# Kernel tuning notes

Hardware: AMD Instinct MI355X
Metric: run time of the kernel (lower is better)

## Reference

```python
import jax, jax.numpy as jnp
import numpy as np


def setup_inputs() -> dict:
    key = jax.random.key(0)
    k_v, k_w = jax.random.split(key)
    L, N, H, D = 2048, 8, 16, 64
    v = jax.random.normal(k_v, (N, L, H, D), dtype=jnp.float32)
    # torch init: self.w.data.uniform_(-0.1, 0.1) overwrites the sorted randn
    w = jax.random.uniform(k_w, (L,), dtype=jnp.float32, minval=-0.1, maxval=0.1)
    return {"v": v, "w": w}


def _toeplitz_bias(w):
    # Faithful to _construnct_bias: p = [flip(w[1:]), w], bias[i, j] = p[L-1 - i + j]
    # which is the symmetric Toeplitz matrix bias[i, j] = w[|i - j|].
    L = w.shape[0]
    idx = jnp.abs(jnp.arange(L)[:, None] - jnp.arange(L)[None, :])  # [L, L]
    return w[idx]


def reference(v, w):
    # PositionalBias._naive
    L = w.shape[0]
    bias = _toeplitz_bias(w)                      # [L, L]
    z_pb = bias.sum(-1).reshape(1, L, 1)          # [1, L, 1]
    pbv = jnp.einsum('nlhd,lj->njhd', v, bias)    # [N, L, H, D]
    return pbv, z_pb
```

## Files before the change

kernel.cpp:

```cpp
#include <hip/hip_runtime.h>
#include <hip/hip_bf16.h>

#define L 2048
#define HD 1024
#define NB 8
#define NT 32
#define PROW 4096

using f32x4 = __attribute__((ext_vector_type(4))) float;
using fl4   = __attribute__((ext_vector_type(4))) float;
using s16x8 = __attribute__((ext_vector_type(8))) short;

__device__ __forceinline__ short f2bf(float f) {
    __hip_bfloat16 h = __float2bfloat16(f);
    short s;
    __builtin_memcpy(&s, &h, 2);
    return s;
}

__device__ __forceinline__ void gload_lds16(const void* g, void* l) {
    __builtin_amdgcn_global_load_lds(
        (const __attribute__((address_space(1))) unsigned int*)g,
        (__attribute__((address_space(3))) unsigned int*)l, 16, 0, 0);
}

__global__ __launch_bounds__(256) void pb_prep(const float* __restrict__ w,
                                               short* __restrict__ p8) {
    int idx = blockIdx.x * 256 + threadIdx.x;
    int s = idx >> 12;
    int x = idx & (PROW - 1);
    int k = x + s;
    short val = 0;
    if (k <= 4094) {
        int d = k - 2047; d = d < 0 ? -d : d;
        val = f2bf(w[d]);
    }
    p8[idx] = val;
}

__global__ __launch_bounds__(256) void pb_vtile(const float* __restrict__ v,
                                                s16x8* __restrict__ vtile) {
    __shared__ __align__(16) short Ts[256 * 64];
    const int kk = blockIdx.x, cm = blockIdx.y, n = blockIdx.z;
    const int l0 = kk * 64, c0 = cm * 256;
    const int t = threadIdx.x;
    const float* vn = v + (size_t)n * L * HD;

    #pragma unroll
    for (int i = 0; i < 16; ++i) {
        int unit = i * 256 + t;
        int l = unit >> 6, cq = unit & 63;
        fl4 x = *(const fl4*)&vn[(size_t)(l0 + l) * HD + c0 + cq * 4];
        int lsub = l & 7, lblk = l >> 3;
        #pragma unroll
        for (int j = 0; j < 4; ++j) {
            int c = cq * 4 + j;
            Ts[c * 64 + ((lblk ^ ((c >> 2) & 7)) << 3) + lsub] = f2bf(x[j]);
        }
    }
    __syncthreads();

    s16x8* outtile = vtile + ((size_t)((n * 4 + cm) * NT + kk)) * 2048;
    #pragma unroll
    for (int i2 = 0; i2 < 8; ++i2) {
        int ci = i2 * 256 + t;
        int nh = ci >> 10, cih = ci & 1023;
        int seg = cih >> 8, o = cih & 255;
        int c = seg * 64 + nh * 32 + (o >> 3), s = o & 7;
        int h = s ^ (c & 7);
        int slot = h ^ ((c >> 2) & 7);
        outtile[ci] = *(const s16x8*)&Ts[c * 64 + slot * 8];
    }
}

__global__ __launch_bounds__(512, 2) void pb_gemm8(const short* __restrict__ p8,
                                                   const short* __restrict__ vtile,
                                                   float* __restrict__ out) {
    __shared__ __align__(16) short lds_[65536];

    const int bid = blockIdx.x;
    const int cmn = bid & 31;
    const int jm  = bid >> 5;
    const int cm  = cmn & 3;
    const int n   = cmn >> 2;
    const int j0 = jm * 256;
    const int c0 = cm * 256;

    const int t = threadIdx.x;
    const int lane = t & 63;
    const int w = t >> 6;
    const int wr = w >> 2, wc = w & 3;
    const int fr = lane & 15, fk = lane >> 4;

    int offA[8], offB[4];
    #pragma unroll
    for (int m = 0; m < 8; ++m) {
        int r = wr * 128 + m * 16 + fr;
        offA[m] = r * 128 + ((fk ^ (r & 7)) << 4);
    }
    #pragma unroll
    for (int nf = 0; nf < 4; ++nf) {
        int c = wc * 64 + nf * 16 + fr;
        offB[nf] = c * 128 + ((fk ^ (c & 7)) << 4);
    }

    auto mkA = [&](int mh, int rho) {
        int dc = rho * 1024 + mh * 512 + w * 64 + lane;
        int r = dc >> 3, s = dc & 7, h = s ^ (r & 7);
        int q = 2047 + h * 8 - j0 - r;
        int srow = q & 7;
        return p8 + srow * PROW + (q - srow);
    };
    const short* srcA0_0 = mkA(0, 0); const short* srcA0_1 = mkA(0, 1);
    const short* srcA1_0 = mkA(1, 0); const short* srcA1_1 = mkA(1, 1);

    const short* vb = vtile + ((size_t)((n * 4 + cm) * NT)) * 2048 * 8;
    const short* srcB0_0 = vb + ((w) * 64 + lane) * 8;
    const short* srcB0_1 = vb + ((w + 8) * 64 + lane) * 8;
    const short* srcB1_0 = vb + (1024 + (w) * 64 + lane) * 8;
    const short* srcB1_1 = vb + (1024 + (w + 8) * 64 + lane) * 8;

    const int dA0 = w * 1024, dA1 = 16384 + w * 1024;
    const int dB0 = 32768 + (w >> 2) * 8192 + (w & 3) * 1024;
    const int dB1 = dB0 + 16384;

#define STAGE_A0(base) { gload_lds16(srcA0_0, (char*)lds_ + (base) + dA0); \
                         gload_lds16(srcA0_1, (char*)lds_ + (base) + dA1); \
                         srcA0_0 += 64; srcA0_1 += 64; }
#define STAGE_A1(base) { gload_lds16(srcA1_0, (char*)lds_ + (base) + 8192 + dA0); \
                         gload_lds16(srcA1_1, (char*)lds_ + (base) + 8192 + dA1); \
                         srcA1_0 += 64; srcA1_1 += 64; }
#define STAGE_B0(base) { gload_lds16(srcB0_0, (char*)lds_ + (base) + dB0); \
                         gload_lds16(srcB0_1, (char*)lds_ + (base) + dB1); \
                         srcB0_0 += 16384; srcB0_1 += 16384; }
#define STAGE_B1(base) { gload_lds16(srcB1_0, (char*)lds_ + (base) + 4096 + dB0); \
                         gload_lds16(srcB1_1, (char*)lds_ + (base) + 4096 + dB1); \
                         srcB1_0 += 16384; srcB1_1 += 16384; }
#define BAR()    asm volatile("s_barrier" ::: "memory")
#define LGKM0()  { asm volatile("s_waitcnt lgkmcnt(0)" ::: "memory"); \
                   __builtin_amdgcn_sched_barrier(0); }
#define VMC4()   asm volatile("s_waitcnt vmcnt(4)" ::: "memory")
#define VMC0()   asm volatile("s_waitcnt vmcnt(0)" ::: "memory")

    STAGE_A0(0); STAGE_A1(0); STAGE_B0(0); STAGE_B1(0);
    STAGE_A0(65536); STAGE_B0(65536);
    VMC4();
    BAR();

    f32x4 acc[8][4] = {};
    s16x8 af[4][2], bf0[2][2], bf1[2][2];

    for (int T = 0; T < NT; ++T) {
        const int par = T & 1;
        const char* bR = (const char*)lds_ + par * 65536;
        const int dstN = (par ^ 1) * 65536;
        const int dstC = par * 65536;

        #pragma unroll
        for (int m = 0; m < 4; ++m) {
            af[m][0] = *(const s16x8*)(bR + offA[m]);
            af[m][1] = *(const s16x8*)(bR + (offA[m] ^ 64));
        }
        #pragma unroll
        for (int nf = 0; nf < 2; ++nf) {
            bf0[nf][0] = *(const s16x8*)(bR + 32768 + offB[nf]);
            bf0[nf][1] = *(const s16x8*)(bR + 32768 + (offB[nf] ^ 64));
        }
        if (T < NT - 1) { STAGE_A1(dstN); }
        BAR(); LGKM0();
        __builtin_amdgcn_s_setprio(1);
        #pragma unroll
        for (int m = 0; m < 4; ++m)
            #pragma unroll
            for (int nf = 0; nf < 2; ++nf)
                #pragma unroll
                for (int ki = 0; ki < 2; ++ki)
                    acc[m][nf] = __builtin_amdgcn_mfma_f32_16x16x32_bf16(
                        af[m][ki], bf0[nf][ki], acc[m][nf], 0, 0, 0);
        __builtin_amdgcn_s_setprio(0);
        BAR();

        #pragma unroll
        for (int nf = 0; nf < 2; ++nf) {
            bf1[nf][0] = *(const s16x8*)(bR + 32768 + offB[2 + nf]);
            bf1[nf][1] = *(const s16x8*)(bR + 32768 + (offB[2 + nf] ^ 64));
        }
        if (T < NT - 1) { STAGE_B1(dstN); }
        BAR(); LGKM0();
        __builtin_amdgcn_s_setprio(1);
        #pragma unroll
        for (int m = 0; m < 4; ++m)
            #pragma unroll
            for (int nf = 0; nf < 2; ++nf)
                #pragma unroll
                for (int ki = 0; ki < 2; ++ki)
                    acc[m][2 + nf] = __builtin_amdgcn_mfma_f32_16x16x32_bf16(
                        af[m][ki], bf1[nf][ki], acc[m][2 + nf], 0, 0, 0);
        __builtin_amdgcn_s_setprio(0);
        BAR();

        #pragma unroll
        for (int m = 0; m < 4; ++m) {
            af[m][0] = *(const s16x8*)(bR + offA[4 + m]);
            af[m][1] = *(const s16x8*)(bR + (offA[4 + m] ^ 64));
        }
        if (T < NT - 2) { STAGE_A0(dstC); }
        BAR(); LGKM0();
        __builtin_amdgcn_s_setprio(1);
        #pragma unroll
        for (int m = 0; m < 4; ++m)
            #pragma unroll
            for (int nf = 0; nf < 2; ++nf)
                #pragma unroll
                for (int ki = 0; ki < 2; ++ki)
                    acc[4 + m][nf] = __builtin_amdgcn_mfma_f32_16x16x32_bf16(
                        af[m][ki], bf0[nf][ki], acc[4 + m][nf], 0, 0, 0);
        __builtin_amdgcn_s_setprio(0);
        BAR();

        if (T < NT - 2) { STAGE_B0(dstC); VMC4(); }
        else            { VMC0(); }
        BAR(); LGKM0();
        __builtin_amdgcn_s_setprio(1);
        #pragma unroll
        for (int m = 0; m < 4; ++m)
            #pragma unroll
            for (int nf = 0; nf < 2; ++nf)
                #pragma unroll
                for (int ki = 0; ki < 2; ++ki)
                    acc[4 + m][2 + nf] = __builtin_amdgcn_mfma_f32_16x16x32_bf16(
                        af[m][ki], bf1[nf][ki], acc[4 + m][2 + nf], 0, 0, 0);
        __builtin_amdgcn_s_setprio(0);
        BAR();
    }

    float* outn = out + (size_t)n * L * HD;
    #pragma unroll
    for (int m = 0; m < 8; ++m) {
        const int row = j0 + wr * 128 + m * 16 + fk * 4;
        #pragma unroll
        for (int nf = 0; nf < 4; ++nf) {
            const int col = c0 + wc * 64 + nf * 16 + fr;
            #pragma unroll
            for (int r = 0; r < 4; ++r)
                outn[(size_t)(row + r) * HD + col] = acc[m][nf][r];
        }
    }
}

__global__ __launch_bounds__(256) void pb_z(const float* __restrict__ w,
                                            float* __restrict__ z) {
    __shared__ float part[256];
    __shared__ float S[L];
    const int t = threadIdx.x;
    float loc[8]; float s = 0.f;
    #pragma unroll
    for (int i = 0; i < 8; ++i) { loc[i] = w[t * 8 + i]; s += loc[i]; }
    part[t] = s;
    __syncthreads();
    if (t == 0) {
        float a = 0.f;
        for (int i = 0; i < 256; ++i) { float tmp = part[i]; part[i] = a; a += tmp; }
    }
    __syncthreads();
    float a = part[t];
    #pragma unroll
    for (int i = 0; i < 8; ++i) { a += loc[i]; S[t * 8 + i] = a; }
    __syncthreads();
    const float w0 = S[0];
    #pragma unroll
    for (int i = 0; i < 8; ++i) {
        int j = t * 8 + i;
        z[j] = S[j] + S[2047 - j] - w0;
    }
}

extern "C" void kernel_launch(void* const* d_in, const int* in_sizes, int n_in,
                              void* d_out, int out_size, void* d_ws, size_t ws_size,
                              hipStream_t stream) {
    const float* v = (const float*)d_in[0];
    const float* w = (const float*)d_in[1];
    float* out = (float*)d_out;

    short* p8    = (short*)d_ws;
    short* vtile = (short*)((char*)d_ws + 65536);

    pb_prep<<<128, 256, 0, stream>>>(w, p8);
    pb_vtile<<<dim3(NT, 4, NB), 256, 0, stream>>>(v, (s16x8*)vtile);
    pb_gemm8<<<256, 512, 0, stream>>>(p8, vtile, out);
    pb_z<<<1, 256, 0, stream>>>(w, out + (size_t)NB * L * HD);
}
```

Baseline: 87.39 us.

## Replace phased LDS pipeline with simple whole-tile double buffering

Drops the four-phase schedule, in which each quarter of the next tile was staged between MFMA groups under explicit barriers, lgkmcnt/vmcnt waits and s_setprio. The new loop issues all eight async global-to-LDS loads for the next tile at the top of each iteration, runs all MFMAs, and ends with a single __syncthreads. This cuts the barrier count per iteration from eight to one and simplifies the code. The cost is coarser overlap, lost wave prioritisation, and reliance on __syncthreads to wait for the async LDS loads to finish.

Result: faster. 81.58 us (-6.6%).

```diff
diff --git a/kernel.cpp b/kernel.cpp
--- a/kernel.cpp
+++ b/kernel.cpp
@@ -124,37 +124,32 @@
     const int dB0 = 32768 + (w >> 2) * 8192 + (w & 3) * 1024;
     const int dB1 = dB0 + 16384;
 
-#define STAGE_A0(base) { gload_lds16(srcA0_0, (char*)lds_ + (base) + dA0); \
-                         gload_lds16(srcA0_1, (char*)lds_ + (base) + dA1); \
-                         srcA0_0 += 64; srcA0_1 += 64; }
-#define STAGE_A1(base) { gload_lds16(srcA1_0, (char*)lds_ + (base) + 8192 + dA0); \
-                         gload_lds16(srcA1_1, (char*)lds_ + (base) + 8192 + dA1); \
-                         srcA1_0 += 64; srcA1_1 += 64; }
-#define STAGE_B0(base) { gload_lds16(srcB0_0, (char*)lds_ + (base) + dB0); \
-                         gload_lds16(srcB0_1, (char*)lds_ + (base) + dB1); \
-                         srcB0_0 += 16384; srcB0_1 += 16384; }
-#define STAGE_B1(base) { gload_lds16(srcB1_0, (char*)lds_ + (base) + 4096 + dB0); \
-                         gload_lds16(srcB1_1, (char*)lds_ + (base) + 4096 + dB1); \
-                         srcB1_0 += 16384; srcB1_1 += 16384; }
-#define BAR()    asm volatile("s_barrier" ::: "memory")
-#define LGKM0()  { asm volatile("s_waitcnt lgkmcnt(0)" ::: "memory"); \
-                   __builtin_amdgcn_sched_barrier(0); }
-#define VMC4()   asm volatile("s_waitcnt vmcnt(4)" ::: "memory")
-#define VMC0()   asm volatile("s_waitcnt vmcnt(0)" ::: "memory")
-
-    STAGE_A0(0); STAGE_A1(0); STAGE_B0(0); STAGE_B1(0);
-    STAGE_A0(65536); STAGE_B0(65536);
-    VMC4();
-    BAR();
+#define STAGE_ALL(base) { \
+    gload_lds16(srcA0_0, (char*)lds_ + (base) + dA0); \
+    gload_lds16(srcA0_1, (char*)lds_ + (base) + dA1); \
+    gload_lds16(srcA1_0, (char*)lds_ + (base) + 8192 + dA0); \
+    gload_lds16(srcA1_1, (char*)lds_ + (base) + 8192 + dA1); \
+    gload_lds16(srcB0_0, (char*)lds_ + (base) + dB0); \
+    gload_lds16(srcB0_1, (char*)lds_ + (base) + dB1); \
+    gload_lds16(srcB1_0, (char*)lds_ + (base) + 4096 + dB0); \
+    gload_lds16(srcB1_1, (char*)lds_ + (base) + 4096 + dB1); \
+    srcA0_0 += 64; srcA0_1 += 64; srcA1_0 += 64; srcA1_1 += 64; \
+    srcB0_0 += 16384; srcB0_1 += 16384; srcB1_0 += 16384; srcB1_1 += 16384; }
+
+    STAGE_ALL(0);
+    __syncthreads();
 
     f32x4 acc[8][4] = {};
-    s16x8 af[4][2], bf0[2][2], bf1[2][2];
 
     for (int T = 0; T < NT; ++T) {
-        const int par = T & 1;
-        const char* bR = (const char*)lds_ + par * 65536;
-        const int dstN = (par ^ 1) * 65536;
-        const int dstC = par * 65536;
+        const char* bR = (const char*)lds_ + (T & 1) * 65536;
+
+        if (T < NT - 1) {
+            const int nb = ((T + 1) & 1) * 65536;
+            STAGE_ALL(nb);
+        }
+
+        s16x8 af[4][2], bf0[2][2], bf1[2][2];
 
         #pragma unroll
         for (int m = 0; m < 4; ++m) {
@@ -166,9 +161,6 @@
             bf0[nf][0] = *(const s16x8*)(bR + 32768 + offB[nf]);
             bf0[nf][1] = *(const s16x8*)(bR + 32768 + (offB[nf] ^ 64));
         }
-        if (T < NT - 1) { STAGE_A1(dstN); }
-        BAR(); LGKM0();
-        __builtin_amdgcn_s_setprio(1);
         #pragma unroll
         for (int m = 0; m < 4; ++m)
             #pragma unroll
@@ -177,17 +169,12 @@
                 for (int ki = 0; ki < 2; ++ki)
                     acc[m][nf] = __builtin_amdgcn_mfma_f32_16x16x32_bf16(
                         af[m][ki], bf0[nf][ki], acc[m][nf], 0, 0, 0);
-        __builtin_amdgcn_s_setprio(0);
-        BAR();
 
         #pragma unroll
         for (int nf = 0; nf < 2; ++nf) {
             bf1[nf][0] = *(const s16x8*)(bR + 32768 + offB[2 + nf]);
             bf1[nf][1] = *(const s16x8*)(bR + 32768 + (offB[2 + nf] ^ 64));
         }
-        if (T < NT - 1) { STAGE_B1(dstN); }
-        BAR(); LGKM0();
-        __builtin_amdgcn_s_setprio(1);
         #pragma unroll
         for (int m = 0; m < 4; ++m)
             #pragma unroll
@@ -196,17 +183,12 @@
                 for (int ki = 0; ki < 2; ++ki)
                     acc[m][2 + nf] = __builtin_amdgcn_mfma_f32_16x16x32_bf16(
                         af[m][ki], bf1[nf][ki], acc[m][2 + nf], 0, 0, 0);
-        __builtin_amdgcn_s_setprio(0);
-        BAR();
 
         #pragma unroll
         for (int m = 0; m < 4; ++m) {
             af[m][0] = *(const s16x8*)(bR + offA[4 + m]);
             af[m][1] = *(const s16x8*)(bR + (offA[4 + m] ^ 64));
         }
-        if (T < NT - 2) { STAGE_A0(dstC); }
-        BAR(); LGKM0();
-        __builtin_amdgcn_s_setprio(1);
         #pragma unroll
         for (int m = 0; m < 4; ++m)
             #pragma unroll
@@ -215,13 +197,7 @@
                 for (int ki = 0; ki < 2; ++ki)
                     acc[4 + m][nf] = __builtin_amdgcn_mfma_f32_16x16x32_bf16(
                         af[m][ki], bf0[nf][ki], acc[4 + m][nf], 0, 0, 0);
-        __builtin_amdgcn_s_setprio(0);
-        BAR();
-
-        if (T < NT - 2) { STAGE_B0(dstC); VMC4(); }
-        else            { VMC0(); }
-        BAR(); LGKM0();
-        __builtin_amdgcn_s_setprio(1);
+
         #pragma unroll
         for (int m = 0; m < 4; ++m)
             #pragma unroll
@@ -230,8 +206,8 @@
                 for (int ki = 0; ki < 2; ++ki)
                     acc[4 + m][2 + nf] = __builtin_amdgcn_mfma_f32_16x16x32_bf16(
                         af[m][ki], bf1[nf][ki], acc[4 + m][2 + nf], 0, 0, 0);
-        __builtin_amdgcn_s_setprio(0);
-        BAR();
+
+        __syncthreads();
     }
 
     float* outn = out + (size_t)n * L * HD;
```
